# Optimization experiments

Hardware: AMD Instinct MI355X
Metric: run time of the kernel (lower is better)

## Reference

```python
import jax, jax.numpy as jnp
import numpy as np

V, O, E, D = 256, 128, 1024, 128
EPS = 1e-5


def setup_inputs() -> dict:
    key = jax.random.key(0)
    ks = jax.random.split(key, 8)
    inp = {}
    inp["obj_vecs"] = jax.random.normal(ks[0], (V, O, D), jnp.float32)
    inp["edges"] = jax.random.randint(ks[1], (V, E, 3), 0, O, dtype=jnp.int64)

    def lin(k, out_d, in_d):  # kaiming-ish init
        return jax.random.normal(k, (out_d, in_d), jnp.float32) * np.float32(np.sqrt(2.0 / in_d))

    i = 2
    for u in range(2):
        inp[f"u{u}_g1"] = jnp.ones((2 * D,), jnp.float32)
        inp[f"u{u}_b1"] = jnp.zeros((2 * D,), jnp.float32)
        inp[f"u{u}_W1"] = lin(ks[i], D, 2 * D); i += 1
        inp[f"u{u}_lb1"] = jnp.zeros((D,), jnp.float32)
        inp[f"u{u}_g2"] = jnp.ones((D,), jnp.float32)
        inp[f"u{u}_b2"] = jnp.zeros((D,), jnp.float32)
        inp[f"u{u}_W2"] = lin(ks[i], D, D); i += 1
        inp[f"u{u}_lb2"] = jnp.zeros((D,), jnp.float32)
    return inp


def _bn_relu(x, g, b):
    # training-mode BatchNorm1d (biased var) -> ReLU, pre-activation
    m = jnp.mean(x, axis=0)
    v = jnp.mean(jnp.square(x - m), axis=0)
    return jax.nn.relu((x - m) * jax.lax.rsqrt(v + EPS) * g + b)


def _gconv(x, s_flat, o_flat, p):
    g1, b1, W1, lb1, g2, b2, W2, lb2 = p
    xf = x.reshape(V * O, -1)
    # gather src/dst node features per edge -> (V*E, 2D)
    node = jnp.concatenate([xf[s_flat], xf[o_flat]], axis=-1)
    edge = _bn_relu(node, g1, b1) @ W1.T + lb1  # (V*E, Dedge)
    # scatter_add pooling onto source nodes, then average by in-count
    pooled = jax.ops.segment_sum(edge, s_flat, num_segments=V * O)
    cnt = jax.ops.segment_sum(jnp.ones((V * E,), edge.dtype), s_flat, num_segments=V * O)
    pooled = pooled / jnp.clip(cnt, 1.0)[:, None]
    out = _bn_relu(pooled, g2, b2) @ W2.T + lb2
    return out.reshape(V, O, -1)


def reference(obj_vecs, edges,
              u0_g1, u0_b1, u0_W1, u0_lb1, u0_g2, u0_b2, u0_W2, u0_lb2,
              u1_g1, u1_b1, u1_W1, u1_lb1, u1_g2, u1_b2, u1_W2, u1_lb2):
    off = (jnp.arange(V, dtype=edges.dtype) * O)[:, None]
    s_flat = (off + edges[:, :, 0]).reshape(-1)
    o_flat = (off + edges[:, :, 2]).reshape(-1)
    x = _gconv(obj_vecs, s_flat, o_flat,
               (u0_g1, u0_b1, u0_W1, u0_lb1, u0_g2, u0_b2, u0_W2, u0_lb2))
    x = _gconv(x, s_flat, o_flat,
               (u1_g1, u1_b1, u1_W1, u1_lb1, u1_g2, u1_b2, u1_W2, u1_lb2))
    return x + obj_vecs  # residual (input_dim == output_dim)
```

## Files before the change

kernel.cpp:

```cpp
#include <hip/hip_runtime.h>

namespace {
constexpr int kV = 256, kO = 128, kE = 1024, kD = 128;
constexpr int kN = kV * kO;
constexpr int kVE = kV * kE;
constexpr float kEps = 1e-5f;
}

typedef __attribute__((ext_vector_type(8))) short bf16x8;
typedef __attribute__((ext_vector_type(8))) unsigned short u16x8;
typedef __attribute__((ext_vector_type(4))) float f32x4;

__device__ __forceinline__ unsigned short f2bf(float x) {
  unsigned u = __float_as_uint(x);
  return (unsigned short)((u + 0x7FFFu + ((u >> 16) & 1u)) >> 16);
}
__device__ __forceinline__ float bf2f(unsigned short h) {
  return __uint_as_float((unsigned)h << 16);
}

__global__ __launch_bounds__(256) void k_init(
    const unsigned int* __restrict__ ew, const float* __restrict__ X,
    int* __restrict__ cnt_s, int* __restrict__ cnt_o,
    unsigned short* __restrict__ Au16, float* __restrict__ p1,
    const float* __restrict__ w1u0, const float* __restrict__ w2u0,
    const float* __restrict__ w1u1, const float* __restrict__ w2u1,
    unsigned short* __restrict__ img0, unsigned short* __restrict__ w2img0,
    unsigned short* __restrict__ img1, unsigned short* __restrict__ w2img1) {
  __shared__ int cnt[kO * kO];
  __shared__ int degS[kO], degO[kO];
  __shared__ int anyodd;
  int t = threadIdx.x;
  if (blockIdx.x >= 256) {
    const float* w1s[2] = {w1u0, w1u1};
    const float* w2s[2] = {w2u0, w2u1};
    unsigned short* img[2] = {img0, img1};
    unsigned short* w2i[2] = {w2img0, w2img1};
    int i0 = (blockIdx.x - 256) * 256 + t, stride = 32 * 256;
#pragma unroll
    for (int u = 0; u < 2; ++u) {
      for (int i = i0; i < kD * 2 * kD; i += stride) {
        int j = i >> 8, k = i & 255;
        int m = k >> 7, kk = k & 127;
        int pos = j * 128 + (kk ^ ((j & 7) << 3));
        float x = w1s[u][i];
        unsigned short hb = f2bf(x);
        img[u][(m * 2 + 0) * 16384 + pos] = hb;
        img[u][(m * 2 + 1) * 16384 + pos] = f2bf(x - bf2f(hb));
      }
      for (int i = i0; i < kD * kD; i += stride) {
        int j = i >> 7, kk = i & 127;
        int pos = j * 128 + (kk ^ ((j & 7) << 3));
        float x = w2s[u][i];
        unsigned short hb = f2bf(x);
        w2i[u][pos] = hb;
        w2i[u][16384 + pos] = f2bf(x - bf2f(hb));
      }
    }
    return;
  }
  int v = blockIdx.x;
  if (t == 0) anyodd = 0;
  for (int i = t; i < kO * kO; i += 256) cnt[i] = 0;
  __syncthreads();
  int base = v * 3072, loc = 0;
  for (int i = t; i < 3072; i += 256) {
    int g = base + i;
    if ((g & 1) && ew[g] != 0u) loc = 1;
  }
  if (loc) atomicOr(&anyodd, 1);
  __syncthreads();
  bool is64 = (anyodd == 0);
  for (int e = t; e < kE; e += 256) {
    long long eb = (long long)(v * kE + e) * 3;
    unsigned s, o;
    if (is64) { s = ew[2 * eb]; o = ew[2 * (eb + 2)]; }
    else      { s = ew[eb];     o = ew[eb + 2]; }
    s &= 127u; o &= 127u;
    atomicAdd(&cnt[s * kO + o], 1);
  }
  __syncthreads();
  unsigned int* A32 = (unsigned int*)(Au16 + (size_t)v * 16384);
  for (int i2 = t; i2 < 8192; i2 += 256) {
    int i = 2 * i2;
    int row = i >> 7, k = i & 127, kg = k >> 3;
    int j = row * 128 + ((kg ^ (row & 7)) << 3) + (k & 7);
    unsigned lo = (unsigned)cnt[i], hi = (unsigned)cnt[i + 1];
    A32[j >> 1] = lo | (hi << 16);
  }
  if (t < kO) {
    int s = 0;
    for (int c = 0; c < kO; ++c) s += cnt[t * kO + ((c + t) & 127)];
    degS[t] = s;
    cnt_s[v * kO + t] = s;
  } else {
    int tc = t - kO;
    int s = 0;
    for (int r = 0; r < kO; ++r) s += cnt[((r + tc) & 127) * kO + tc];
    degO[tc] = s;
    cnt_o[v * kO + tc] = s;
  }
  __syncthreads();
  int dq = (t & 31) * 4, rg = t >> 5;
  float acc[4][4];
#pragma unroll
  for (int a = 0; a < 4; ++a)
#pragma unroll
    for (int j = 0; j < 4; ++j) acc[a][j] = 0.f;
  for (int k = 0; k < 16; ++k) {
    int row = rg + k * 8;
    float4 xv = *(const float4*)(X + ((size_t)v * kO + row) * kD + dq);
    float wsv = (float)degS[row], wov = (float)degO[row];
    float xs[4] = {xv.x, xv.y, xv.z, xv.w};
#pragma unroll
    for (int j = 0; j < 4; ++j) {
      acc[0][j] += wsv * xs[j];
      acc[1][j] += wsv * xs[j] * xs[j];
      acc[2][j] += wov * xs[j];
      acc[3][j] += wov * xs[j] * xs[j];
    }
  }
  float* red = (float*)cnt;
  for (int st = 0; st < 4; ++st) {
    __syncthreads();
#pragma unroll
    for (int j = 0; j < 4; ++j) red[rg * 128 + dq + j] = acc[st][j];
    __syncthreads();
    if (t < 128) {
      float s = 0.f;
#pragma unroll
      for (int g = 0; g < 8; ++g) s += red[g * 128 + t];
      p1[((size_t)v * 4 + st) * 128 + t] = s;
    }
  }
}

__global__ __launch_bounds__(256) void k_fin1(
    const float* __restrict__ p1, const float* __restrict__ g1,
    const float* __restrict__ b1, float* __restrict__ coef, int nslots) {
  __shared__ double sS[256], sQ[256];
  int c = blockIdx.x, t = threadIdx.x;
  int half = c >> 7, d = c & 127;
  double S = 0.0, Q = 0.0;
  for (int b = t; b < nslots; b += 256) {
    S += (double)p1[((size_t)b * 4 + half * 2 + 0) * 128 + d];
    Q += (double)p1[((size_t)b * 4 + half * 2 + 1) * 128 + d];
  }
  sS[t] = S; sQ[t] = Q;
  __syncthreads();
  for (int s = 128; s > 0; s >>= 1) {
    if (t < s) { sS[t] += sS[t + s]; sQ[t] += sQ[t + s]; }
    __syncthreads();
  }
  if (t == 0) {
    double m = sS[0] / (double)kVE;
    double var = sQ[0] / (double)kVE - m * m;
    float a = g1[c] / sqrtf((float)var + kEps);
    float beta = b1[c] - (float)m * a;
    coef[half * 256 + d] = a;
    coef[half * 256 + 128 + d] = beta;
  }
}

__global__ __launch_bounds__(512, 2) void k_fused1(
    const float* __restrict__ X, const unsigned short* __restrict__ w1img,
    const float* __restrict__ coef, const unsigned short* __restrict__ Au16,
    const int* __restrict__ cnt_s, const float* __restrict__ lb1,
    float* __restrict__ pooled, float* __restrict__ p2) {
  __shared__ __align__(16) unsigned short Wl[4][16384];
  int t = threadIdx.x, v = blockIdx.x;
  int lane = t & 63, wid = t >> 6;
  int wr = wid * 16, lrow = lane & 15, lkc = lane >> 4;
  int arow = wr + lrow;
#pragma unroll
  for (int a = 0; a < 4; ++a)
#pragma unroll
    for (int i = 0; i < 4; ++i)
      __builtin_amdgcn_global_load_lds(
          (const unsigned int*)((const char*)(w1img + a * 16384) +
                                wid * 4096 + i * 1024 + lane * 16),
          (unsigned int*)((char*)Wl[a] + wid * 4096 + i * 1024), 16, 0, 0);
  u16x8 au[4];
#pragma unroll
  for (int ks = 0; ks < 4; ++ks) {
    int kg = ks * 4 + lkc;
    au[ks] = *(const u16x8*)(Au16 + (size_t)v * 16384 + arow * 128 +
                             ((kg ^ (arow & 7)) << 3));
  }
  bf16x8 hsH[4], hsL[4], hoH[4], hoL[4];
#pragma unroll
  for (int ks = 0; ks < 4; ++ks) {
    int kb = ks * 32 + lkc * 8;
    float4 x0 = *(const float4*)(X + ((size_t)v * kO + arow) * kD + kb);
    float4 x1 = *(const float4*)(X + ((size_t)v * kO + arow) * kD + kb + 4);
    float4 aS0 = *(const float4*)(coef + kb),       aS1 = *(const float4*)(coef + kb + 4);
    float4 bS0 = *(const float4*)(coef + 128 + kb), bS1 = *(const float4*)(coef + 128 + kb + 4);
    float4 aO0 = *(const float4*)(coef + 256 + kb), aO1 = *(const float4*)(coef + 256 + kb + 4);
    float4 bO0 = *(const float4*)(coef + 384 + kb), bO1 = *(const float4*)(coef + 384 + kb + 4);
    float xs[8] = {x0.x, x0.y, x0.z, x0.w, x1.x, x1.y, x1.z, x1.w};
    float as[8] = {aS0.x, aS0.y, aS0.z, aS0.w, aS1.x, aS1.y, aS1.z, aS1.w};
    float bs[8] = {bS0.x, bS0.y, bS0.z, bS0.w, bS1.x, bS1.y, bS1.z, bS1.w};
    float ao[8] = {aO0.x, aO0.y, aO0.z, aO0.w, aO1.x, aO1.y, aO1.z, aO1.w};
    float bo[8] = {bO0.x, bO0.y, bO0.z, bO0.w, bO1.x, bO1.y, bO1.z, bO1.w};
#pragma unroll
    for (int e = 0; e < 8; ++e) {
      float hs = fmaxf(as[e] * xs[e] + bs[e], 0.f);
      float ho = fmaxf(ao[e] * xs[e] + bo[e], 0.f);
      unsigned short h1 = f2bf(hs);
      hsH[ks][e] = (short)h1;
      hsL[ks][e] = (short)f2bf(hs - bf2f(h1));
      unsigned short h2 = f2bf(ho);
      hoH[ks][e] = (short)h2;
      hoL[ks][e] = (short)f2bf(ho - bf2f(h2));
    }
  }
  __syncthreads();
  f32x4 accS[8], accO[8];
#pragma unroll
  for (int j = 0; j < 8; ++j) {
    accS[j] = (f32x4){0.f, 0.f, 0.f, 0.f};
    accO[j] = (f32x4){0.f, 0.f, 0.f, 0.f};
  }
#pragma unroll
  for (int ks = 0; ks < 4; ++ks) {
    int kb = ks * 32 + lkc * 8;
#pragma unroll
    for (int jg = 0; jg < 8; ++jg) {
      int j = jg * 16 + lrow;
      int idx = j * 128 + (kb ^ ((j & 7) << 3));
      bf16x8 bsh = *(const bf16x8*)(&Wl[0][idx]);
      bf16x8 bsl = *(const bf16x8*)(&Wl[1][idx]);
      bf16x8 boh = *(const bf16x8*)(&Wl[2][idx]);
      bf16x8 bol = *(const bf16x8*)(&Wl[3][idx]);
      accS[jg] = __builtin_amdgcn_mfma_f32_16x16x32_bf16(hsH[ks], bsh, accS[jg], 0, 0, 0);
      accS[jg] = __builtin_amdgcn_mfma_f32_16x16x32_bf16(hsH[ks], bsl, accS[jg], 0, 0, 0);
      accS[jg] = __builtin_amdgcn_mfma_f32_16x16x32_bf16(hsL[ks], bsh, accS[jg], 0, 0, 0);
      accO[jg] = __builtin_amdgcn_mfma_f32_16x16x32_bf16(hoH[ks], boh, accO[jg], 0, 0, 0);
      accO[jg] = __builtin_amdgcn_mfma_f32_16x16x32_bf16(hoH[ks], bol, accO[jg], 0, 0, 0);
      accO[jg] = __builtin_amdgcn_mfma_f32_16x16x32_bf16(hoL[ks], boh, accO[jg], 0, 0, 0);
    }
  }
  __syncthreads();
#pragma unroll
  for (int jg = 0; jg < 8; ++jg) {
    int d = jg * 16 + lrow;
#pragma unroll
    for (int q = 0; q < 4; ++q) {
      int o = wr + lkc * 4 + q;
      int addr = d * 128 + (o ^ ((d & 7) << 3));
      float vv = accO[jg][q];
      unsigned short h = f2bf(vv);
      Wl[0][addr] = h;
      Wl[1][addr] = f2bf(vv - bf2f(h));
    }
  }
  __syncthreads();
  f32x4 accP[8];
#pragma unroll
  for (int j = 0; j < 8; ++j) accP[j] = (f32x4){0.f, 0.f, 0.f, 0.f};
#pragma unroll
  for (int ks = 0; ks < 4; ++ks) {
    int kb = ks * 32 + lkc * 8;
    bf16x8 pah, pal;
#pragma unroll
    for (int e = 0; e < 8; ++e) {
      float c = (float)au[ks][e];
      unsigned short hb = f2bf(c);
      pah[e] = (short)hb;
      pal[e] = (short)f2bf(c - bf2f(hb));
    }
#pragma unroll
    for (int jg = 0; jg < 8; ++jg) {
      int d = jg * 16 + lrow;
      int qi = d * 128 + (kb ^ ((d & 7) << 3));
      bf16x8 qh = *(const bf16x8*)(&Wl[0][qi]), ql = *(const bf16x8*)(&Wl[1][qi]);
      accP[jg] = __builtin_amdgcn_mfma_f32_16x16x32_bf16(pah, qh, accP[jg], 0, 0, 0);
      accP[jg] = __builtin_amdgcn_mfma_f32_16x16x32_bf16(pah, ql, accP[jg], 0, 0, 0);
      accP[jg] = __builtin_amdgcn_mfma_f32_16x16x32_bf16(pal, qh, accP[jg], 0, 0, 0);
    }
  }
  float lb[8];
#pragma unroll
  for (int jg = 0; jg < 8; ++jg) lb[jg] = lb1[jg * 16 + lrow];
  float sm[8], sq[8];
#pragma unroll
  for (int jg = 0; jg < 8; ++jg) { sm[jg] = 0.f; sq[jg] = 0.f; }
#pragma unroll
  for (int q = 0; q < 4; ++q) {
    int row = wr + lkc * 4 + q;
    size_t n = (size_t)v * kO + row;
    int cnt = cnt_s[n];
    float inv = (cnt > 0) ? 1.f / (float)cnt : 0.f;
#pragma unroll
    for (int jg = 0; jg < 8; ++jg) {
      int col = jg * 16 + lrow;
      float pv = 0.f;
      if (cnt > 0) pv = accS[jg][q] + lb[jg] + accP[jg][q] * inv;
      pooled[n * kD + col] = pv;
      sm[jg] += pv; sq[jg] += pv * pv;
    }
  }
  float* red = (float*)Wl[2];
  int slot = wid * 4 + lkc;
#pragma unroll
  for (int jg = 0; jg < 8; ++jg) red[slot * 128 + jg * 16 + lrow] = sm[jg];
  __syncthreads();
  if (t < 128) {
    float s = 0.f;
#pragma unroll
    for (int g = 0; g < 32; ++g) s += red[g * 128 + t];
    p2[((size_t)v * 2 + 0) * 128 + t] = s;
  }
  __syncthreads();
#pragma unroll
  for (int jg = 0; jg < 8; ++jg) red[slot * 128 + jg * 16 + lrow] = sq[jg];
  __syncthreads();
  if (t < 128) {
    float s = 0.f;
#pragma unroll
    for (int g = 0; g < 32; ++g) s += red[g * 128 + t];
    p2[((size_t)v * 2 + 1) * 128 + t] = s;
  }
}

__global__ __launch_bounds__(256) void k_fin2(
    const float* __restrict__ p2, const float* __restrict__ g2,
    const float* __restrict__ b2, float* __restrict__ coef2) {
  __shared__ double sS[256], sQ[256];
  int d = blockIdx.x, t = threadIdx.x;
  double S = (double)p2[((size_t)t * 2 + 0) * 128 + d];
  double Q = (double)p2[((size_t)t * 2 + 1) * 128 + d];
  sS[t] = S; sQ[t] = Q;
  __syncthreads();
  for (int s = 128; s > 0; s >>= 1) {
    if (t < s) { sS[t] += sS[t + s]; sQ[t] += sQ[t + s]; }
    __syncthreads();
  }
  if (t == 0) {
    double m = sS[0] / (double)kN, var = sQ[0] / (double)kN - m * m;
    float a = g2[d] / sqrtf((float)var + kEps);
    float beta = b2[d] - (float)m * a;
    coef2[d] = a; coef2[128 + d] = beta;
  }
}

template <int STATS>
__global__ __launch_bounds__(512, 2) void k_gemm(
    const float* __restrict__ X, const unsigned short* __restrict__ w2img,
    const float* __restrict__ coefA, const float* __restrict__ coefB,
    float* __restrict__ Y, const float* __restrict__ bias, const float* __restrict__ resid,
    const int* __restrict__ cnt_s, const int* __restrict__ cnt_o,
    float* __restrict__ p1out) {
  __shared__ __align__(16) unsigned short Wl[2][16384];
  int t = threadIdx.x, rb = blockIdx.x;
  int lane = t & 63, wid = t >> 6;
  int wr = wid * 16, lrow = lane & 15, lkc = lane >> 4;
  int arow = wr + lrow;
#pragma unroll
  for (int a = 0; a < 2; ++a)
#pragma unroll
    for (int i = 0; i < 4; ++i)
      __builtin_amdgcn_global_load_lds(
          (const unsigned int*)((const char*)(w2img + a * 16384) +
                                wid * 4096 + i * 1024 + lane * 16),
          (unsigned int*)((char*)Wl[a] + wid * 4096 + i * 1024), 16, 0, 0);
  bf16x8 ahH[4], ahL[4];
#pragma unroll
  for (int ks = 0; ks < 4; ++ks) {
    int kb = ks * 32 + lkc * 8;
    float4 x0 = *(const float4*)(X + ((size_t)rb * kO + arow) * kD + kb);
    float4 x1 = *(const float4*)(X + ((size_t)rb * kO + arow) * kD + kb + 4);
    float4 a0 = *(const float4*)(coefA + kb), a1 = *(const float4*)(coefA + kb + 4);
    float4 b0 = *(const float4*)(coefB + kb), b1 = *(const float4*)(coefB + kb + 4);
    float xs[8] = {x0.x, x0.y, x0.z, x0.w, x1.x, x1.y, x1.z, x1.w};
    float as[8] = {a0.x, a0.y, a0.z, a0.w, a1.x, a1.y, a1.z, a1.w};
    float bs[8] = {b0.x, b0.y, b0.z, b0.w, b1.x, b1.y, b1.z, b1.w};
#pragma unroll
    for (int e = 0; e < 8; ++e) {
      float h = fmaxf(as[e] * xs[e] + bs[e], 0.f);
      unsigned short hb = f2bf(h);
      ahH[ks][e] = (short)hb;
      ahL[ks][e] = (short)f2bf(h - bf2f(hb));
    }
  }
  __syncthreads();
  f32x4 acc[8];
#pragma unroll
  for (int j = 0; j < 8; ++j) acc[j] = (f32x4){0.f, 0.f, 0.f, 0.f};
#pragma unroll
  for (int ks = 0; ks < 4; ++ks) {
    int kb = ks * 32 + lkc * 8;
#pragma unroll
    for (int jg = 0; jg < 8; ++jg) {
      int j = jg * 16 + lrow;
      int idx = j * 128 + (kb ^ ((j & 7) << 3));
      bf16x8 bh = *(const bf16x8*)(&Wl[0][idx]);
      bf16x8 bl = *(const bf16x8*)(&Wl[1][idx]);
      acc[jg] = __builtin_amdgcn_mfma_f32_16x16x32_bf16(ahH[ks], bh, acc[jg], 0, 0, 0);
      acc[jg] = __builtin_amdgcn_mfma_f32_16x16x32_bf16(ahH[ks], bl, acc[jg], 0, 0, 0);
      acc[jg] = __builtin_amdgcn_mfma_f32_16x16x32_bf16(ahL[ks], bh, acc[jg], 0, 0, 0);
    }
  }
  float s0[8], s1[8], s2[8], s3[8];
  if (STATS) {
#pragma unroll
    for (int jg = 0; jg < 8; ++jg) { s0[jg] = 0.f; s1[jg] = 0.f; s2[jg] = 0.f; s3[jg] = 0.f; }
  }
  float wsr[4], wor[4];
  if (STATS) {
#pragma unroll
    for (int q = 0; q < 4; ++q) {
      int n = rb * kO + wr + lkc * 4 + q;
      wsr[q] = (float)cnt_s[n]; wor[q] = (float)cnt_o[n];
    }
  }
#pragma unroll
  for (int jg = 0; jg < 8; ++jg) {
    int col = jg * 16 + lrow;
    float bcol = bias ? bias[col] : 0.f;
#pragma unroll
    for (int q = 0; q < 4; ++q) {
      int row = wr + lkc * 4 + q;
      size_t n = (size_t)rb * kO + row;
      float vv = acc[jg][q] + bcol;
      if (resid) vv += resid[n * kD + col];
      Y[n * kD + col] = vv;
      if (STATS) {
        s0[jg] += wsr[q] * vv; s1[jg] += wsr[q] * vv * vv;
        s2[jg] += wor[q] * vv; s3[jg] += wor[q] * vv * vv;
      }
    }
  }
  if (STATS) {
    __syncthreads();
    float* red = (float*)Wl;
    int slot = wid * 4 + lkc;
#pragma unroll
    for (int jg = 0; jg < 8; ++jg) {
      int col = jg * 16 + lrow;
      red[0 * 4096 + slot * 128 + col] = s0[jg];
      red[1 * 4096 + slot * 128 + col] = s1[jg];
      red[2 * 4096 + slot * 128 + col] = s2[jg];
      red[3 * 4096 + slot * 128 + col] = s3[jg];
    }
    __syncthreads();
    if (t < 128) {
#pragma unroll
      for (int st = 0; st < 4; ++st) {
        float s = 0.f;
#pragma unroll
        for (int g = 0; g < 32; ++g) s += red[st * 4096 + g * 128 + t];
        p1out[((size_t)rb * 4 + st) * 128 + t] = s;
      }
    }
  }
}

extern "C" void kernel_launch(void* const* d_in, const int* in_sizes, int n_in,
                              void* d_out, int out_size, void* d_ws, size_t ws_size,
                              hipStream_t stream) {
  (void)in_sizes; (void)n_in; (void)out_size; (void)ws_size;
  const float* obj = (const float*)d_in[0];
  const unsigned int* ew = (const unsigned int*)d_in[1];
  const float* prm[2][8];
  for (int u = 0; u < 2; ++u)
    for (int p = 0; p < 8; ++p) prm[u][p] = (const float*)d_in[2 + u * 8 + p];

  char* ws = (char*)d_ws;
  size_t off = 0;
  auto carve = [&](size_t bytes) -> char* {
    char* p = ws + off;
    off = (off + bytes + 255) & ~(size_t)255;
    return p;
  };
  int* cnt_s = (int*)carve((size_t)kN * 4);
  int* cnt_o = (int*)carve((size_t)kN * 4);
  unsigned short* Au16 = (unsigned short*)carve((size_t)kV * 16384 * 2);
  float* p1 = (float*)carve((size_t)256 * 4 * 128 * 4);
  float* p2 = (float*)carve((size_t)kV * 2 * 128 * 4);
  float* coef1 = (float*)carve(512 * 4);
  float* coef2 = (float*)carve(256 * 4);
  unsigned short *w1img[2], *w2img[2];
  for (int u = 0; u < 2; ++u) {
    w1img[u] = (unsigned short*)carve((size_t)4 * 16384 * 2);
    w2img[u] = (unsigned short*)carve((size_t)2 * 16384 * 2);
  }
  float* pooled = (float*)carve((size_t)kN * kD * 4);
  float* x2 = (float*)carve((size_t)kN * kD * 4);

  k_init<<<288, 256, 0, stream>>>(ew, obj, cnt_s, cnt_o, Au16, p1,
                                  prm[0][2], prm[0][6], prm[1][2], prm[1][6],
                                  w1img[0], w2img[0], w1img[1], w2img[1]);

  float* outp = (float*)d_out;
  k_fin1<<<256, 256, 0, stream>>>(p1, prm[0][0], prm[0][1], coef1, 256);
  k_fused1<<<kV, 512, 0, stream>>>(obj, w1img[0], coef1, Au16,
                                   cnt_s, prm[0][3], pooled, p2);
  k_fin2<<<128, 256, 0, stream>>>(p2, prm[0][4], prm[0][5], coef2);
  k_gemm<1><<<kV, 512, 0, stream>>>(pooled, w2img[0], coef2, coef2 + 128,
                                    x2, prm[0][7], nullptr, cnt_s, cnt_o, p1);
  k_fin1<<<256, 256, 0, stream>>>(p1, prm[1][0], prm[1][1], coef1, 256);
  k_fused1<<<kV, 512, 0, stream>>>(x2, w1img[1], coef1, Au16,
                                   cnt_s, prm[1][3], pooled, p2);
  k_fin2<<<128, 256, 0, stream>>>(p2, prm[1][4], prm[1][5], coef2);
  k_gemm<0><<<kV, 512, 0, stream>>>(pooled, w2img[1], coef2, coef2 + 128,
                                    outp, prm[1][7], obj, nullptr, nullptr, nullptr);
}
```

Before: 102.5 us.

## Fuse edge GEMM, BN2 finalize and node GEMM into one cooperative kernel

Merges k_fused1, k_fin2 and k_gemm into a single cooperative kernel per unit. The pooled tile stays in LDS with an XOR swizzle, and a grid-wide sync separates the pooled-stats reduction from the second GEMM, with each block recomputing the BN2 coefficients from p2. This removes two kernel launches per unit and the global write and read of the pooled tensor. In exchange it needs a grid sync, where all 256 blocks must be co-resident, and every block does a redundant reduction over p2.

```diff
diff --git a/kernel.cpp b/kernel.cpp
--- a/kernel.cpp
+++ b/kernel.cpp
@@ -1,4 +1,7 @@
 #include <hip/hip_runtime.h>
+#include <hip/hip_cooperative_groups.h>
+
+namespace cg = cooperative_groups;
 
 namespace {
 constexpr int kV = 256, kO = 128, kE = 1024, kD = 128;
@@ -137,15 +140,12 @@
 
 __global__ __launch_bounds__(256) void k_fin1(
     const float* __restrict__ p1, const float* __restrict__ g1,
-    const float* __restrict__ b1, float* __restrict__ coef, int nslots) {
+    const float* __restrict__ b1, float* __restrict__ coef) {
   __shared__ double sS[256], sQ[256];
   int c = blockIdx.x, t = threadIdx.x;
   int half = c >> 7, d = c & 127;
-  double S = 0.0, Q = 0.0;
-  for (int b = t; b < nslots; b += 256) {
-    S += (double)p1[((size_t)b * 4 + half * 2 + 0) * 128 + d];
-    Q += (double)p1[((size_t)b * 4 + half * 2 + 1) * 128 + d];
-  }
+  double S = (double)p1[((size_t)t * 4 + half * 2 + 0) * 128 + d];
+  double Q = (double)p1[((size_t)t * 4 + half * 2 + 1) * 128 + d];
   sS[t] = S; sQ[t] = Q;
   __syncthreads();
   for (int s = 128; s > 0; s >>= 1) {
@@ -162,12 +162,20 @@
   }
 }
 
-__global__ __launch_bounds__(512, 2) void k_fused1(
-    const float* __restrict__ X, const unsigned short* __restrict__ w1img,
-    const float* __restrict__ coef, const unsigned short* __restrict__ Au16,
-    const int* __restrict__ cnt_s, const float* __restrict__ lb1,
-    float* __restrict__ pooled, float* __restrict__ p2) {
+template <int STATS>
+__global__ __launch_bounds__(512, 2) void k_unit(
+    const float* __restrict__ X,
+    const unsigned short* __restrict__ w1img,
+    const unsigned short* __restrict__ w2img,
+    const float* __restrict__ coef1, const unsigned short* __restrict__ Au16,
+    const int* __restrict__ cnt_s, const int* __restrict__ cnt_o,
+    const float* __restrict__ lb1, const float* __restrict__ g2,
+    const float* __restrict__ b2, const float* __restrict__ bias2,
+    const float* __restrict__ resid,
+    float* __restrict__ p2, float* __restrict__ Y, float* __restrict__ p1out) {
   __shared__ __align__(16) unsigned short Wl[4][16384];
+  __shared__ double scd[2][512];
+  __shared__ float cf[2][128];
   int t = threadIdx.x, v = blockIdx.x;
   int lane = t & 63, wid = t >> 6;
   int wr = wid * 16, lrow = lane & 15, lkc = lane >> 4;
@@ -193,10 +201,10 @@
     int kb = ks * 32 + lkc * 8;
     float4 x0 = *(const float4*)(X + ((size_t)v * kO + arow) * kD + kb);
     float4 x1 = *(const float4*)(X + ((size_t)v * kO + arow) * kD + kb + 4);
-    float4 aS0 = *(const float4*)(coef + kb),       aS1 = *(const float4*)(coef + kb + 4);
-    float4 bS0 = *(const float4*)(coef + 128 + kb), bS1 = *(const float4*)(coef + 128 + kb + 4);
-    float4 aO0 = *(const float4*)(coef + 256 + kb), aO1 = *(const float4*)(coef + 256 + kb + 4);
-    float4 bO0 = *(const float4*)(coef + 384 + kb), bO1 = *(const float4*)(coef + 384 + kb + 4);
+    float4 aS0 = *(const float4*)(coef1 + kb),       aS1 = *(const float4*)(coef1 + kb + 4);
+    float4 bS0 = *(const float4*)(coef1 + 128 + kb), bS1 = *(const float4*)(coef1 + 128 + kb + 4);
+    float4 aO0 = *(const float4*)(coef1 + 256 + kb), aO1 = *(const float4*)(coef1 + 256 + kb + 4);
+    float4 bO0 = *(const float4*)(coef1 + 384 + kb), bO1 = *(const float4*)(coef1 + 384 + kb + 4);
     float xs[8] = {x0.x, x0.y, x0.z, x0.w, x1.x, x1.y, x1.z, x1.w};
     float as[8] = {aS0.x, aS0.y, aS0.z, aS0.w, aS1.x, aS1.y, aS1.z, aS1.w};
     float bs[8] = {bS0.x, bS0.y, bS0.z, bS0.w, bS1.x, bS1.y, bS1.z, bS1.w};
@@ -279,6 +287,9 @@
       accP[jg] = __builtin_amdgcn_mfma_f32_16x16x32_bf16(pal, qh, accP[jg], 0, 0, 0);
     }
   }
+  __syncthreads();
+  float* plds = (float*)Wl[2];
+  float* red  = (float*)Wl[0];
   float lb[8];
 #pragma unroll
   for (int jg = 0; jg < 8; ++jg) lb[jg] = lb1[jg * 16 + lrow];
@@ -296,11 +307,10 @@
       int col = jg * 16 + lrow;
       float pv = 0.f;
       if (cnt > 0) pv = accS[jg][q] + lb[jg] + accP[jg][q] * inv;
-      pooled[n * kD + col] = pv;
+      plds[row * 128 + (col ^ ((row & 7) << 2))] = pv;
       sm[jg] += pv; sq[jg] += pv * pv;
     }
   }
-  float* red = (float*)Wl[2];
   int slot = wid * 4 + lkc;
 #pragma unroll
   for (int jg = 0; jg < 8; ++jg) red[slot * 128 + jg * 16 + lrow] = sm[jg];
@@ -321,41 +331,8 @@
     for (int g = 0; g < 32; ++g) s += red[g * 128 + t];
     p2[((size_t)v * 2 + 1) * 128 + t] = s;
   }
-}
-
-__global__ __launch_bounds__(256) void k_fin2(
-    const float* __restrict__ p2, const float* __restrict__ g2,
-    const float* __restrict__ b2, float* __restrict__ coef2) {
-  __shared__ double sS[256], sQ[256];
-  int d = blockIdx.x, t = threadIdx.x;
-  double S = (double)p2[((size_t)t * 2 + 0) * 128 + d];
-  double Q = (double)p2[((size_t)t * 2 + 1) * 128 + d];
-  sS[t] = S; sQ[t] = Q;
-  __syncthreads();
-  for (int s = 128; s > 0; s >>= 1) {
-    if (t < s) { sS[t] += sS[t + s]; sQ[t] += sQ[t + s]; }
-    __syncthreads();
-  }
-  if (t == 0) {
-    double m = sS[0] / (double)kN, var = sQ[0] / (double)kN - m * m;
-    float a = g2[d] / sqrtf((float)var + kEps);
-    float beta = b2[d] - (float)m * a;
-    coef2[d] = a; coef2[128 + d] = beta;
-  }
-}
-
-template <int STATS>
-__global__ __launch_bounds__(512, 2) void k_gemm(
-    const float* __restrict__ X, const unsigned short* __restrict__ w2img,
-    const float* __restrict__ coefA, const float* __restrict__ coefB,
-    float* __restrict__ Y, const float* __restrict__ bias, const float* __restrict__ resid,
-    const int* __restrict__ cnt_s, const int* __restrict__ cnt_o,
-    float* __restrict__ p1out) {
-  __shared__ __align__(16) unsigned short Wl[2][16384];
-  int t = threadIdx.x, rb = blockIdx.x;
-  int lane = t & 63, wid = t >> 6;
-  int wr = wid * 16, lrow = lane & 15, lkc = lane >> 4;
-  int arow = wr + lrow;
+  __threadfence();
+  cg::this_grid().sync();
 #pragma unroll
   for (int a = 0; a < 2; ++a)
 #pragma unroll
@@ -364,26 +341,41 @@
           (const unsigned int*)((const char*)(w2img + a * 16384) +
                                 wid * 4096 + i * 1024 + lane * 16),
           (unsigned int*)((char*)Wl[a] + wid * 4096 + i * 1024), 16, 0, 0);
+  {
+    int d = t & 127, g = t >> 7;
+    double S = 0.0, Q = 0.0;
+    for (int vv = g * 64; vv < g * 64 + 64; ++vv) {
+      S += (double)p2[((size_t)vv * 2 + 0) * 128 + d];
+      Q += (double)p2[((size_t)vv * 2 + 1) * 128 + d];
+    }
+    scd[0][t] = S; scd[1][t] = Q;
+  }
+  __syncthreads();
+  if (t < 128) {
+    double St = scd[0][t] + scd[0][128 + t] + scd[0][256 + t] + scd[0][384 + t];
+    double Qt = scd[1][t] + scd[1][128 + t] + scd[1][256 + t] + scd[1][384 + t];
+    double m = St / (double)kN, var = Qt / (double)kN - m * m;
+    float a2 = g2[t] / sqrtf((float)var + kEps);
+    cf[0][t] = a2;
+    cf[1][t] = b2[t] - (float)m * a2;
+  }
+  __syncthreads();
+  int sw = (arow & 7) << 2;
   bf16x8 ahH[4], ahL[4];
 #pragma unroll
   for (int ks = 0; ks < 4; ++ks) {
     int kb = ks * 32 + lkc * 8;
-    float4 x0 = *(const float4*)(X + ((size_t)rb * kO + arow) * kD + kb);
-    float4 x1 = *(const float4*)(X + ((size_t)rb * kO + arow) * kD + kb + 4);
-    float4 a0 = *(const float4*)(coefA + kb), a1 = *(const float4*)(coefA + kb + 4);
-    float4 b0 = *(const float4*)(coefB + kb), b1 = *(const float4*)(coefB + kb + 4);
-    float xs[8] = {x0.x, x0.y, x0.z, x0.w, x1.x, x1.y, x1.z, x1.w};
-    float as[8] = {a0.x, a0.y, a0.z, a0.w, a1.x, a1.y, a1.z, a1.w};
-    float bs[8] = {b0.x, b0.y, b0.z, b0.w, b1.x, b1.y, b1.z, b1.w};
+    float4 p0 = *(const float4*)&plds[arow * 128 + (kb ^ sw)];
+    float4 p1v = *(const float4*)&plds[arow * 128 + ((kb + 4) ^ sw)];
+    float ps[8] = {p0.x, p0.y, p0.z, p0.w, p1v.x, p1v.y, p1v.z, p1v.w};
 #pragma unroll
     for (int e = 0; e < 8; ++e) {
-      float h = fmaxf(as[e] * xs[e] + bs[e], 0.f);
+      float h = fmaxf(cf[0][kb + e] * ps[e] + cf[1][kb + e], 0.f);
       unsigned short hb = f2bf(h);
       ahH[ks][e] = (short)hb;
       ahL[ks][e] = (short)f2bf(h - bf2f(hb));
     }
   }
-  __syncthreads();
   f32x4 acc[8];
 #pragma unroll
   for (int j = 0; j < 8; ++j) acc[j] = (f32x4){0.f, 0.f, 0.f, 0.f};
@@ -410,18 +402,18 @@
   if (STATS) {
 #pragma unroll
     for (int q = 0; q < 4; ++q) {
-      int n = rb * kO + wr + lkc * 4 + q;
+      int n = v * kO + wr + lkc * 4 + q;
       wsr[q] = (float)cnt_s[n]; wor[q] = (float)cnt_o[n];
     }
   }
 #pragma unroll
   for (int jg = 0; jg < 8; ++jg) {
     int col = jg * 16 + lrow;
-    float bcol = bias ? bias[col] : 0.f;
+    float bcol = bias2[col];
 #pragma unroll
     for (int q = 0; q < 4; ++q) {
       int row = wr + lkc * 4 + q;
-      size_t n = (size_t)rb * kO + row;
+      size_t n = (size_t)v * kO + row;
       float vv = acc[jg][q] + bcol;
       if (resid) vv += resid[n * kD + col];
       Y[n * kD + col] = vv;
@@ -433,15 +425,14 @@
   }
   if (STATS) {
     __syncthreads();
-    float* red = (float*)Wl;
-    int slot = wid * 4 + lkc;
+    float* red4 = (float*)Wl[0];
 #pragma unroll
     for (int jg = 0; jg < 8; ++jg) {
       int col = jg * 16 + lrow;
-      red[0 * 4096 + slot * 128 + col] = s0[jg];
-      red[1 * 4096 + slot * 128 + col] = s1[jg];
-      red[2 * 4096 + slot * 128 + col] = s2[jg];
-      red[3 * 4096 + slot * 128 + col] = s3[jg];
+      red4[0 * 4096 + slot * 128 + col] = s0[jg];
+      red4[1 * 4096 + slot * 128 + col] = s1[jg];
+      red4[2 * 4096 + slot * 128 + col] = s2[jg];
+      red4[3 * 4096 + slot * 128 + col] = s3[jg];
     }
     __syncthreads();
     if (t < 128) {
@@ -449,8 +440,8 @@
       for (int st = 0; st < 4; ++st) {
         float s = 0.f;
 #pragma unroll
-        for (int g = 0; g < 32; ++g) s += red[st * 4096 + g * 128 + t];
-        p1out[((size_t)rb * 4 + st) * 128 + t] = s;
+        for (int g = 0; g < 32; ++g) s += red4[st * 4096 + g * 128 + t];
+        p1out[((size_t)v * 4 + st) * 128 + t] = s;
       }
     }
   }
@@ -479,30 +470,48 @@
   float* p1 = (float*)carve((size_t)256 * 4 * 128 * 4);
   float* p2 = (float*)carve((size_t)kV * 2 * 128 * 4);
   float* coef1 = (float*)carve(512 * 4);
-  float* coef2 = (float*)carve(256 * 4);
   unsigned short *w1img[2], *w2img[2];
   for (int u = 0; u < 2; ++u) {
     w1img[u] = (unsigned short*)carve((size_t)4 * 16384 * 2);
     w2img[u] = (unsigned short*)carve((size_t)2 * 16384 * 2);
   }
-  float* pooled = (float*)carve((size_t)kN * kD * 4);
   float* x2 = (float*)carve((size_t)kN * kD * 4);
+  float* outp = (float*)d_out;
 
   k_init<<<288, 256, 0, stream>>>(ew, obj, cnt_s, cnt_o, Au16, p1,
                                   prm[0][2], prm[0][6], prm[1][2], prm[1][6],
                                   w1img[0], w2img[0], w1img[1], w2img[1]);
 
-  float* outp = (float*)d_out;
-  k_fin1<<<256, 256, 0, stream>>>(p1, prm[0][0], prm[0][1], coef1, 256);
-  k_fused1<<<kV, 512, 0, stream>>>(obj, w1img[0], coef1, Au16,
-                                   cnt_s, prm[0][3], pooled, p2);
-  k_fin2<<<128, 256, 0, stream>>>(p2, prm[0][4], prm[0][5], coef2);
-  k_gemm<1><<<kV, 512, 0, stream>>>(pooled, w2img[0], coef2, coef2 + 128,
-                                    x2, prm[0][7], nullptr, cnt_s, cnt_o, p1);
-  k_fin1<<<256, 256, 0, stream>>>(p1, prm[1][0], prm[1][1], coef1, 256);
-  k_fused1<<<kV, 512, 0, stream>>>(x2, w1img[1], coef1, Au16,
-                                   cnt_s, prm[1][3], pooled, p2);
-  k_fin2<<<128, 256, 0, stream>>>(p2, prm[1][4], prm[1][5], coef2);
-  k_gemm<0><<<kV, 512, 0, stream>>>(pooled, w2img[1], coef2, coef2 + 128,
-                                    outp, prm[1][7], obj, nullptr, nullptr, nullptr);
-}
+  k_fin1<<<256, 256, 0, stream>>>(p1, prm[0][0], prm[0][1], coef1);
+  {
+    const float* X = obj;
+    const unsigned short *wi = w1img[0], *w2i = w2img[0];
+    const float *c1 = coef1;
+    const unsigned short* Au = Au16;
+    const int *cs = cnt_s, *co = cnt_o;
+    const float *l1 = prm[0][3], *g2p = prm[0][4], *b2p = prm[0][5], *bi2 = prm[0][7];
+    const float* rs = nullptr;
+    float *p2p = p2, *Yp = x2, *p1p = p1;
+    void* args[] = {(void*)&X, (void*)&wi, (void*)&w2i, (void*)&c1, (void*)&Au,
+                    (void*)&cs, (void*)&co, (void*)&l1, (void*)&g2p, (void*)&b2p,
+                    (void*)&bi2, (void*)&rs, (void*)&p2p, (void*)&Yp, (void*)&p1p};
+    hipLaunchCooperativeKernel((const void*)k_unit<1>, dim3(kV), dim3(512),
+                               args, 0, stream);
+  }
+  k_fin1<<<256, 256, 0, stream>>>(p1, prm[1][0], prm[1][1], coef1);
+  {
+    const float* X = x2;
+    const unsigned short *wi = w1img[1], *w2i = w2img[1];
+    const float *c1 = coef1;
+    const unsigned short* Au = Au16;
+    const int *cs = cnt_s, *co = cnt_o;
+    const float *l1 = prm[1][3], *g2p = prm[1][4], *b2p = prm[1][5], *bi2 = prm[1][7];
+    const float* rs = obj;
+    float *p2p = p2, *Yp = outp, *p1p = p1;
+    void* args[] = {(void*)&X, (void*)&wi, (void*)&w2i, (void*)&c1, (void*)&Au,
+                    (void*)&cs, (void*)&co, (void*)&l1, (void*)&g2p, (void*)&b2p,
+                    (void*)&bi2, (void*)&rs, (void*)&p2p, (void*)&Yp, (void*)&p1p};
+    hipLaunchCooperativeKernel((const void*)k_unit<0>, dim3(kV), dim3(512),
+                               args, 0, stream);
+  }
+}
```

New measurement: 284.7 us, median of 3. +177.8%, slower.
